# Kernel optimization log

Hardware: AMD Instinct MI355X
Metric: run time of the kernel (lower is better)

Reference implementation:

```python
import jax, jax.numpy as jnp
import numpy as np

N_ACTIVE = 32

def setup_inputs() -> dict:
    key = jax.random.key(0)
    ks = jax.random.split(key, 6)
    B, T, D, G, GD = 4, 2048, 2048, 4096, 256
    x = jax.random.normal(ks[0], (B, T, D), jnp.float32)
    Wc = jax.random.normal(ks[1], (G, D), jnp.float32) * (D ** -0.5)   # context_proj weight
    temperature = jnp.array(1.0, jnp.float32)
    genes = jax.random.normal(ks[2], (G, GD), jnp.float32) * 0.02      # dna_bank gene table
    Wd = jax.random.normal(ks[3], (D, GD), jnp.float32) * (GD ** -0.5) # gene_to_down weight
    Wu = jax.random.normal(ks[4], (D, GD), jnp.float32) * 0.02         # gene_to_up (zeros in init; random for testing)
    norm_w = jnp.ones((D,), jnp.float32)                               # RMSNorm weight
    scale = jnp.array(0.1, jnp.float32)
    return {"x": x, "Wc": Wc, "temperature": temperature, "genes": genes,
            "Wd": Wd, "Wu": Wu, "norm_w": norm_w, "scale": scale}

def reference(x, Wc, temperature, genes, Wd, Wu, norm_w, scale):
    # RMSNorm (torch default eps = finfo(dtype).eps, learnable elementwise weight)
    eps = jnp.finfo(x.dtype).eps
    xn = x * jax.lax.rsqrt(jnp.mean(x * x, axis=-1, keepdims=True) + eps) * norm_w
    # Expression: router logits over gene bank, temperature clamped at 0.1
    logits = jnp.einsum('btd,gd->btg', xn, Wc) / jnp.clip(temperature, 0.1)
    # top-k + scatter(-inf) + softmax == softmax over top-k values, zeros elsewhere
    top_vals, top_idx = jax.lax.top_k(logits, N_ACTIVE)        # (B,T,K)
    expr_w = jax.nn.softmax(top_vals, axis=-1)                 # (B,T,K)
    # dna_bank.express: weighted combination of genes. Only top-k entries are
    # nonzero, so gather + weighted sum is mathematically identical to the
    # dense (B,T,G)@(G,GD) combine the original materializes.
    expressed = jnp.einsum('btk,btkc->btc', expr_w, genes[top_idx])  # (B,T,GD)
    down = jnp.tanh(jnp.einsum('btc,dc->btd', expressed, Wd))
    up = jnp.einsum('btc,dc->btd', expressed, Wu)
    return down * xn * up * scale
```

## Files before the change

kernel.cpp:

```cpp
#include <hip/hip_runtime.h>
#include <math.h>

#define M_TOK 8192
#define D_DIM 2048
#define G_GENES 4096
#define GD_DIM 256
#define KSEL 32
#define NCAND 40
#define NSLICE 8

typedef float f32x4 __attribute__((ext_vector_type(4)));
typedef short bf16x8 __attribute__((ext_vector_type(8)));

__device__ __forceinline__ void async_copy16(const void* g, void* lds) {
  __builtin_amdgcn_global_load_lds((const __attribute__((address_space(1))) void*)g,
                                   (__attribute__((address_space(3))) void*)lds, 16, 0, 0);
}

__device__ __forceinline__ unsigned short f2bf(float f) {
  unsigned int u = __float_as_uint(f);
  unsigned int r = (u + 0x7fffu + ((u >> 16) & 1u)) >> 16;
  return (unsigned short)r;
}
__device__ __forceinline__ float bf2f(unsigned short h) {
  return __uint_as_float(((unsigned int)h) << 16);
}

__global__ __launch_bounds__(256) void k1_rmsnorm(const float* __restrict__ x,
                                                  const float* __restrict__ nw,
                                                  float* __restrict__ r_out,
                                                  unsigned short* __restrict__ xn_bf) {
  int t = blockIdx.x, tid = threadIdx.x;
  const float4* xr = (const float4*)(x + (size_t)t * D_DIM);
  float4 a = xr[tid], b = xr[tid + 256];
  double ss = (double)a.x*a.x + (double)a.y*a.y + (double)a.z*a.z + (double)a.w*a.w
            + (double)b.x*b.x + (double)b.y*b.y + (double)b.z*b.z + (double)b.w*b.w;
  for (int off = 32; off; off >>= 1) ss += __shfl_down(ss, off);
  __shared__ double sred[4];
  __shared__ float rshare;
  int lane = tid & 63, wv = tid >> 6;
  if (lane == 0) sred[wv] = ss;
  __syncthreads();
  if (tid == 0) {
    double tot = sred[0] + sred[1] + sred[2] + sred[3];
    float r = (float)(1.0 / sqrt(tot / (double)D_DIM + 1.1920928955078125e-7));
    rshare = r; r_out[t] = r;
  }
  __syncthreads();
  float r = rshare;
  const float4* nw4 = (const float4*)nw;
  float4 na = nw4[tid], nb = nw4[tid + 256];
  ushort4 oa, ob;
  oa.x = f2bf(a.x * r * na.x); oa.y = f2bf(a.y * r * na.y);
  oa.z = f2bf(a.z * r * na.z); oa.w = f2bf(a.w * r * na.w);
  ob.x = f2bf(b.x * r * nb.x); ob.y = f2bf(b.y * r * nb.y);
  ob.z = f2bf(b.z * r * nb.z); ob.w = f2bf(b.w * r * nb.w);
  ushort4* o4 = (ushort4*)(xn_bf + (size_t)t * D_DIM);
  o4[tid] = oa; o4[tid + 256] = ob;
}

__global__ __launch_bounds__(256) void k2_cvt(const float* __restrict__ w,
                                              unsigned short* __restrict__ wb) {
  size_t i = (size_t)blockIdx.x * 256 + threadIdx.x;
  const float4* w4 = (const float4*)w;
  float4 a = w4[2*i], b = w4[2*i+1];
  ushort4 oa, ob;
  oa.x = f2bf(a.x); oa.y = f2bf(a.y); oa.z = f2bf(a.z); oa.w = f2bf(a.w);
  ob.x = f2bf(b.x); ob.y = f2bf(b.y); ob.z = f2bf(b.z); ob.w = f2bf(b.w);
  ((ushort4*)wb)[2*i] = oa; ((ushort4*)wb)[2*i+1] = ob;
}

__global__ __launch_bounds__(256) void k2b_split(const float* __restrict__ wd,
                                                 const float* __restrict__ wu,
                                                 unsigned short* __restrict__ wdh,
                                                 unsigned short* __restrict__ wdl,
                                                 unsigned short* __restrict__ wuh,
                                                 unsigned short* __restrict__ wul) {
  const float* src = blockIdx.y ? wu : wd;
  unsigned short* dh = blockIdx.y ? wuh : wdh;
  unsigned short* dl = blockIdx.y ? wul : wdl;
  size_t i = (size_t)blockIdx.x * 256 + threadIdx.x;
  float4 v = ((const float4*)src)[i];
  ushort4 h, l;
  h.x = f2bf(v.x); l.x = f2bf(v.x - bf2f(h.x));
  h.y = f2bf(v.y); l.y = f2bf(v.y - bf2f(h.y));
  h.z = f2bf(v.z); l.z = f2bf(v.z - bf2f(h.z));
  h.w = f2bf(v.w); l.w = f2bf(v.w - bf2f(h.w));
  ((ushort4*)dh)[i] = h;
  ((ushort4*)dl)[i] = l;
}

__global__ __launch_bounds__(512, 1) void k3_gemm_logits(const unsigned short* __restrict__ A,
                                                         const unsigned short* __restrict__ B,
                                                         unsigned short* __restrict__ C) {
  __shared__ unsigned short As[4][256 * 32];
  __shared__ unsigned short Bs[4][256 * 32];
  const int tid = threadIdx.x;
  const int lane = tid & 63, wv = tid >> 6;
  const int wm = wv >> 2, wn = wv & 3;
  int lin = blockIdx.x;
  int swz = (lin & 7) * 64 + (lin >> 3);
  const int bm = swz & 31, bn = swz >> 5;

  const int grow = lane >> 2;
  const int gslot = (lane & 3) ^ ((lane >> 3) & 3);
  const unsigned short* agp = A + (size_t)(bm * 256 + wv * 32 + grow) * D_DIM + gslot * 8;
  const unsigned short* bgp = B + (size_t)(bn * 256 + wv * 32 + grow) * D_DIM + gslot * 8;
  const int fr = lane & 15;
  const int sw8 = (((lane >> 4) ^ ((lane >> 1) & 3))) * 8;

  f32x4 acc[8][4];
#pragma unroll
  for (int m = 0; m < 8; ++m)
#pragma unroll
    for (int n = 0; n < 4; ++n) acc[m][n] = (f32x4){0.f, 0.f, 0.f, 0.f};

#define STAGE_A3(t_) { const int b_ = (t_) & 3; const int kt_ = (t_) * 32;          \
    async_copy16(agp + kt_,              &As[b_][(wv * 32) * 32]);                   \
    async_copy16(agp + kt_ + 16 * D_DIM, &As[b_][(wv * 32 + 16) * 32]); }
#define STAGE_B3(t_) { const int b_ = (t_) & 3; const int kt_ = (t_) * 32;          \
    async_copy16(bgp + kt_,              &Bs[b_][(wv * 32) * 32]);                   \
    async_copy16(bgp + kt_ + 16 * D_DIM, &Bs[b_][(wv * 32 + 16) * 32]); }

#define READ_FRAGS(fa_, fb_, c_) {                                                   \
    const unsigned short* as_ = As[c_];                                              \
    const unsigned short* bs_ = Bs[c_];                                              \
    _Pragma("unroll") for (int n = 0; n < 4; ++n)                                    \
      fb_[n] = *(const bf16x8*)&bs_[(wn * 64 + n * 16 + fr) * 32 + sw8];             \
    _Pragma("unroll") for (int m = 0; m < 8; ++m)                                    \
      fa_[m] = *(const bf16x8*)&as_[(wm * 128 + m * 16 + fr) * 32 + sw8]; }

#define DO_MFMA(fa_, fb_) {                                                          \
    _Pragma("unroll") for (int m = 0; m < 4; ++m)                                    \
      _Pragma("unroll") for (int n = 0; n < 4; ++n)                                  \
        acc[m][n] = __builtin_amdgcn_mfma_f32_16x16x32_bf16(fa_[m], fb_[n], acc[m][n], 0, 0, 0); \
    _Pragma("unroll") for (int m = 0; m < 4; ++m)                                    \
      _Pragma("unroll") for (int n = 0; n < 4; ++n)                                  \
        acc[m + 4][n] = __builtin_amdgcn_mfma_f32_16x16x32_bf16(fa_[m + 4], fb_[n], acc[m + 4][n], 0, 0, 0); }

#define BODY(t_, CFA, CFB, NFA, NFB) {                                               \
    if ((t_) + 3 < 64) { STAGE_A3((t_) + 3); STAGE_B3((t_) + 3); }                   \
    READ_FRAGS(NFA, NFB, ((t_) + 1) & 3);                                            \
    asm volatile("s_waitcnt lgkmcnt(12)" ::: "memory");                              \
    __builtin_amdgcn_sched_barrier(0);                                               \
    __builtin_amdgcn_s_setprio(1);                                                   \
    DO_MFMA(CFA, CFB);                                                               \
    __builtin_amdgcn_s_setprio(0);                                                   \
    if ((t_) <= 60)      { asm volatile("s_waitcnt vmcnt(4)" ::: "memory"); }        \
    else if ((t_) == 61) { asm volatile("s_waitcnt vmcnt(0)" ::: "memory"); }        \
    __builtin_amdgcn_s_barrier(); }

  STAGE_A3(0); STAGE_B3(0);
  STAGE_A3(1); STAGE_B3(1);
  STAGE_A3(2); STAGE_B3(2);
  asm volatile("s_waitcnt vmcnt(4)" ::: "memory");
  __builtin_amdgcn_s_barrier();

  bf16x8 faA[8], fbA[4], faB[8], fbB[4];
  READ_FRAGS(faA, fbA, 0);

#pragma unroll 1
  for (int t = 0; t < 62; t += 2) {
    BODY(t,     faA, fbA, faB, fbB);
    BODY(t + 1, faB, fbB, faA, fbA);
  }
  BODY(62, faA, fbA, faB, fbB);
  asm volatile("s_waitcnt lgkmcnt(0)" ::: "memory");
  __builtin_amdgcn_sched_barrier(0);
  DO_MFMA(faB, fbB);

#undef BODY
#undef DO_MFMA
#undef READ_FRAGS
#undef STAGE_A3
#undef STAGE_B3

#pragma unroll
  for (int m = 0; m < 8; ++m)
#pragma unroll
    for (int n = 0; n < 4; ++n)
#pragma unroll
      for (int j = 0; j < 4; ++j) {
        int row = bm * 256 + wm * 128 + m * 16 + (lane >> 4) * 4 + j;
        int col = bn * 256 + wn * 64 + n * 16 + fr;
        C[(size_t)row * G_GENES + col] = f2bf(acc[m][n][j]);
      }
}

__global__ __launch_bounds__(256) void k4_topk(const unsigned short* __restrict__ L,
                                               int* __restrict__ cand) {
  int wv = threadIdx.x >> 6, lane = threadIdx.x & 63;
  int t = blockIdx.x * 4 + wv;
  const unsigned short* lp = L + (size_t)t * G_GENES;
  unsigned kp[32];
#pragma unroll
  for (int i = 0; i < 8; ++i) {
    uint4 raw = *(const uint4*)(lp + i * 512 + lane * 8);
    unsigned rr[4] = {raw.x, raw.y, raw.z, raw.w};
#pragma unroll
    for (int q = 0; q < 4; ++q) {
      unsigned r = rr[q];
      unsigned s = (r >> 15) & 0x00010001u;
      unsigned xm = 0x80008000u | (s * 0x7FFFu);
      kp[i * 4 + q] = r ^ xm;
    }
  }
  unsigned lo = 0, hi = 65536;
  while (hi - lo > 1u) {
    unsigned mid = (lo + hi) >> 1;
    int c = 0;
#pragma unroll
    for (int q = 0; q < 32; ++q) {
      c += __popcll(__ballot((kp[q] & 0xFFFFu) >= mid));
      c += __popcll(__ballot((kp[q] >> 16) >= mid));
    }
    if (c >= NCAND) lo = mid; else hi = mid;
  }
  const unsigned T = lo;
  unsigned long long below = (1ull << lane) - 1ull;
  int* outp = cand + (size_t)t * NCAND;
  int cnt = 0;
#pragma unroll
  for (int q = 0; q < 32; ++q) {
#pragma unroll
    for (int h = 0; h < 2; ++h) {
      unsigned key = h ? (kp[q] >> 16) : (kp[q] & 0xFFFFu);
      bool pred = key > T;
      unsigned long long m = __ballot(pred);
      if (pred) {
        int pos = cnt + (int)__popcll(m & below);
        outp[pos] = (q >> 2) * 512 + lane * 8 + (q & 3) * 2 + h;
      }
      cnt += (int)__popcll(m);
    }
  }
#pragma unroll 1
  for (int q = 0; q < 32 && cnt < NCAND; ++q) {
#pragma unroll
    for (int h = 0; h < 2; ++h) {
      unsigned key = h ? (kp[q] >> 16) : (kp[q] & 0xFFFFu);
      bool pred = key == T;
      unsigned long long m = __ballot(pred);
      if (pred) {
        int pos = cnt + (int)__popcll(m & below);
        if (pos < NCAND)
          outp[pos] = (q >> 2) * 512 + lane * 8 + (q & 3) * 2 + h;
      }
      cnt += (int)__popcll(m);
    }
  }
}

__global__ __launch_bounds__(256) void k5a_partial(const float* __restrict__ x,
                                                   const float* __restrict__ r,
                                                   const float* __restrict__ nw,
                                                   const float* __restrict__ Wc,
                                                   const int* __restrict__ cand,
                                                   double* __restrict__ part) {
  int bid = blockIdx.x;
  int slice = bid & 7;
  int group = bid >> 3;
  int wv = threadIdx.x >> 6, lane = threadIdx.x & 63;
  const int dbase = slice * 256;
  float4 nv = *(const float4*)(nw + dbase + lane * 4);
  bool b0 = (lane & 1) != 0, b1 = (lane & 2) != 0, b2 = (lane & 4) != 0;
#pragma unroll 1
  for (int tt = 0; tt < 2; ++tt) {
    int t = group * 8 + wv * 2 + tt;
    float rr = r[t];
    float4 xv = *(const float4*)(x + (size_t)t * D_DIM + dbase + lane * 4);
    float4 xl;
    xl.x = xv.x * rr * nv.x;
    xl.y = xv.y * rr * nv.y;
    xl.z = xv.z * rr * nv.z;
    xl.w = xv.w * rr * nv.w;
    int myg = cand[t * NCAND + (lane < NCAND ? lane : 0)];
    double* outp = part + ((size_t)t * NSLICE + slice) * NCAND;
#pragma unroll 1
    for (int j0 = 0; j0 < NCAND; j0 += 8) {
      float4 w[8];
#pragma unroll
      for (int c = 0; c < 8; ++c) {
        int g = __shfl(myg, j0 + c);
        w[c] = *(const float4*)(Wc + (size_t)g * D_DIM + dbase + lane * 4);
      }
      double s[8];
#pragma unroll
      for (int c = 0; c < 8; ++c)
        s[c] = ((double)xl.x * (double)w[c].x + (double)xl.y * (double)w[c].y)
             + ((double)xl.z * (double)w[c].z + (double)xl.w * (double)w[c].w);
      double u01 = b0 ? s[1] : s[0], t01 = b0 ? s[0] : s[1];
      double u23 = b0 ? s[3] : s[2], t23 = b0 ? s[2] : s[3];
      double u45 = b0 ? s[5] : s[4], t45 = b0 ? s[4] : s[5];
      double u67 = b0 ? s[7] : s[6], t67 = b0 ? s[6] : s[7];
      u01 += __shfl_xor(t01, 1);
      u23 += __shfl_xor(t23, 1);
      u45 += __shfl_xor(t45, 1);
      u67 += __shfl_xor(t67, 1);
      double v03 = b1 ? u23 : u01, t03 = b1 ? u01 : u23;
      double v47 = b1 ? u67 : u45, t47 = b1 ? u45 : u67;
      v03 += __shfl_xor(t03, 2);
      v47 += __shfl_xor(t47, 2);
      double wsum = b2 ? v47 : v03, t07 = b2 ? v03 : v47;
      wsum += __shfl_xor(t07, 4);
      wsum += __shfl_xor(wsum, 8);
      wsum += __shfl_xor(wsum, 16);
      wsum += __shfl_xor(wsum, 32);
      if (lane < 8) outp[j0 + lane] = wsum;
    }
  }
}

__global__ __launch_bounds__(256) void k6_express(const double* __restrict__ part,
                                                  const int* __restrict__ cand,
                                                  const float* __restrict__ genes,
                                                  const float* __restrict__ temp,
                                                  unsigned short* __restrict__ e_hi,
                                                  unsigned short* __restrict__ e_lo) {
  int t = blockIdx.x, tid = threadIdx.x;
  __shared__ double sval[NCAND];
  __shared__ int sidx[NCAND];
  __shared__ float sw[NCAND];
  float tclamp = fmaxf(temp[0], 0.1f);
  if (tid < NCAND) {
    const double* pp = part + (size_t)t * NSLICE * NCAND + tid;
    double v = 0.0;
#pragma unroll
    for (int s = 0; s < NSLICE; ++s) v += pp[s * NCAND];
    sval[tid] = v / (double)tclamp;
    sidx[tid] = cand[(size_t)t * NCAND + tid];
  }
  __syncthreads();
  if (tid < 64) {
    double v = (tid < NCAND) ? sval[tid] : -1.0e300;
    int gi = (tid < NCAND) ? sidx[tid] : 0x7fffffff;
    int rank = 0;
    for (int j = 0; j < NCAND; ++j) {
      double vj = sval[j]; int gj = sidx[j];
      if (vj > v || (vj == v && gj < gi)) rank++;
    }
    bool sel = (tid < NCAND) && (rank < KSEL);
    double vs = sel ? v : -1.0e300;
    double mx = vs;
    for (int off = 32; off; off >>= 1) { double o = __shfl_xor(mx, off); mx = fmax(mx, o); }
    double e = sel ? exp(v - mx) : 0.0;
    double ssum = e;
    for (int off = 32; off; off >>= 1) ssum += __shfl_xor(ssum, off);
    if (tid < NCAND) sw[tid] = (float)(e / ssum);
  }
  __syncthreads();
  float a0 = 0.f, a1 = 0.f, a2 = 0.f, a3 = 0.f;
#pragma unroll
  for (int k = 0; k < NCAND; k += 4) {
    a0 += sw[k]     * genes[(size_t)sidx[k]     * GD_DIM + tid];
    a1 += sw[k + 1] * genes[(size_t)sidx[k + 1] * GD_DIM + tid];
    a2 += sw[k + 2] * genes[(size_t)sidx[k + 2] * GD_DIM + tid];
    a3 += sw[k + 3] * genes[(size_t)sidx[k + 3] * GD_DIM + tid];
  }
  float acc = (a0 + a1) + (a2 + a3);
  unsigned short h = f2bf(acc);
  unsigned short l = f2bf(acc - bf2f(h));
  e_hi[(size_t)t * GD_DIM + tid] = h;
  e_lo[(size_t)t * GD_DIM + tid] = l;
}

__global__ __launch_bounds__(512, 1) void k7_mfma(const unsigned short* __restrict__ e_hi,
                                                  const unsigned short* __restrict__ e_lo,
                                                  const unsigned short* __restrict__ wdh,
                                                  const unsigned short* __restrict__ wdl,
                                                  const unsigned short* __restrict__ wuh,
                                                  const unsigned short* __restrict__ wul,
                                                  const float* __restrict__ x,
                                                  const float* __restrict__ r,
                                                  const float* __restrict__ nw,
                                                  const float* __restrict__ scale_p,
                                                  float* __restrict__ out) {
  __shared__ unsigned short L[3][6][128 * 32];
  const int tid = threadIdx.x;
  const int lane = tid & 63, wv = tid >> 6;
  const int wm = wv >> 2, wn = wv & 3;
  int lin = blockIdx.x;
  int swz = (lin & 7) * 128 + (lin >> 3);
  const int bm = swz & 63, bn = swz >> 6;

  const int grow = lane >> 2;
  const int gslot = (lane & 3) ^ ((lane >> 3) & 3);
  const int goff = gslot * 8;
  const unsigned short* ehp = e_hi + (size_t)(bm * 128 + wv * 16 + grow) * GD_DIM + goff;
  const unsigned short* elp = e_lo + (size_t)(bm * 128 + wv * 16 + grow) * GD_DIM + goff;
  const unsigned short* dhp = wdh + (size_t)(bn * 128 + wv * 16 + grow) * GD_DIM + goff;
  const unsigned short* dlp = wdl + (size_t)(bn * 128 + wv * 16 + grow) * GD_DIM + goff;
  const unsigned short* uhp = wuh + (size_t)(bn * 128 + wv * 16 + grow) * GD_DIM + goff;
  const unsigned short* ulp = wul + (size_t)(bn * 128 + wv * 16 + grow) * GD_DIM + goff;
  const int ldst = (wv * 16) * 32;

  const int fr = lane & 15;
  const int sw8 = ((lane >> 4) ^ ((lane >> 1) & 3)) * 8;

  f32x4 accD[4][2], accU[4][2];
#pragma unroll
  for (int m = 0; m < 4; ++m)
#pragma unroll
    for (int n = 0; n < 2; ++n) {
      accD[m][n] = (f32x4){0.f, 0.f, 0.f, 0.f};
      accU[m][n] = (f32x4){0.f, 0.f, 0.f, 0.f};
    }

#define STAGE7(t_) if ((t_) < 8) { const int b_ = (t_) % 3; const int kt_ = (t_) * 32; \
    async_copy16(ehp + kt_, &L[b_][0][ldst]); \
    async_copy16(elp + kt_, &L[b_][1][ldst]); \
    async_copy16(dhp + kt_, &L[b_][2][ldst]); \
    async_copy16(dlp + kt_, &L[b_][3][ldst]); \
    async_copy16(uhp + kt_, &L[b_][4][ldst]); \
    async_copy16(ulp + kt_, &L[b_][5][ldst]); }

  STAGE7(0); STAGE7(1);
  asm volatile("s_waitcnt vmcnt(6)" ::: "memory");
  __builtin_amdgcn_s_barrier();

#pragma unroll 1
  for (int t = 0; t < 8; ++t) {
    const int b = t % 3;
    bf16x8 fah[4], fal[4], fh[2], fl[2];
#pragma unroll
    for (int m = 0; m < 4; ++m) {
      int off = (wm * 64 + m * 16 + fr) * 32 + sw8;
      fah[m] = *(const bf16x8*)&L[b][0][off];
      fal[m] = *(const bf16x8*)&L[b][1][off];
    }
#pragma unroll
    for (int n = 0; n < 2; ++n) {
      int off = (wn * 32 + n * 16 + fr) * 32 + sw8;
      fh[n] = *(const bf16x8*)&L[b][2][off];
      fl[n] = *(const bf16x8*)&L[b][3][off];
    }
    STAGE7(t + 2);
    __builtin_amdgcn_s_barrier();
    asm volatile("s_waitcnt lgkmcnt(0)" ::: "memory");
    __builtin_amdgcn_sched_barrier(0);
    __builtin_amdgcn_s_setprio(1);
#pragma unroll
    for (int m = 0; m < 4; ++m)
#pragma unroll
      for (int n = 0; n < 2; ++n) {
        accD[m][n] = __builtin_amdgcn_mfma_f32_16x16x32_bf16(fah[m], fh[n], accD[m][n], 0, 0, 0);
        accD[m][n] = __builtin_amdgcn_mfma_f32_16x16x32_bf16(fah[m], fl[n], accD[m][n], 0, 0, 0);
        accD[m][n] = __builtin_amdgcn_mfma_f32_16x16x32_bf16(fal[m], fh[n], accD[m][n], 0, 0, 0);
      }
    __builtin_amdgcn_s_setprio(0);
    __builtin_amdgcn_s_barrier();
#pragma unroll
    for (int n = 0; n < 2; ++n) {
      int off = (wn * 32 + n * 16 + fr) * 32 + sw8;
      fh[n] = *(const bf16x8*)&L[b][4][off];
      fl[n] = *(const bf16x8*)&L[b][5][off];
    }
    __builtin_amdgcn_s_barrier();
    asm volatile("s_waitcnt lgkmcnt(0)" ::: "memory");
    __builtin_amdgcn_sched_barrier(0);
    __builtin_amdgcn_s_setprio(1);
#pragma unroll
    for (int m = 0; m < 4; ++m)
#pragma unroll
      for (int n = 0; n < 2; ++n) {
        accU[m][n] = __builtin_amdgcn_mfma_f32_16x16x32_bf16(fah[m], fh[n], accU[m][n], 0, 0, 0);
        accU[m][n] = __builtin_amdgcn_mfma_f32_16x16x32_bf16(fah[m], fl[n], accU[m][n], 0, 0, 0);
        accU[m][n] = __builtin_amdgcn_mfma_f32_16x16x32_bf16(fal[m], fh[n], accU[m][n], 0, 0, 0);
      }
    __builtin_amdgcn_s_setprio(0);
    if (t <= 5)      { asm volatile("s_waitcnt vmcnt(6)" ::: "memory"); }
    else if (t == 6) { asm volatile("s_waitcnt vmcnt(0)" ::: "memory"); }
    __builtin_amdgcn_s_barrier();
  }
#undef STAGE7

  float sc = scale_p[0];
#pragma unroll
  for (int m = 0; m < 4; ++m)
#pragma unroll
    for (int j = 0; j < 4; ++j) {
      int token = bm * 128 + wm * 64 + m * 16 + (lane >> 4) * 4 + j;
      float rr = r[token];
#pragma unroll
      for (int n = 0; n < 2; ++n) {
        int d = bn * 128 + wn * 32 + n * 16 + fr;
        float xn = x[(size_t)token * D_DIM + d] * rr * nw[d];
        out[(size_t)token * D_DIM + d] = tanhf(accD[m][n][j]) * xn * accU[m][n][j] * sc;
      }
    }
}

extern "C" void kernel_launch(void* const* d_in, const int* in_sizes, int n_in,
                              void* d_out, int out_size, void* d_ws, size_t ws_size,
                              hipStream_t stream) {
  const float* x       = (const float*)d_in[0];
  const float* Wc      = (const float*)d_in[1];
  const float* temp    = (const float*)d_in[2];
  const float* genes   = (const float*)d_in[3];
  const float* Wd      = (const float*)d_in[4];
  const float* Wu      = (const float*)d_in[5];
  const float* nw      = (const float*)d_in[6];
  const float* scale_p = (const float*)d_in[7];

  char* ws = (char*)d_ws;
  float* r_buf          = (float*)ws;
  unsigned short* xn_bf = (unsigned short*)(ws + 65536);
  unsigned short* wc_bf = (unsigned short*)(ws + 65536 + (size_t)M_TOK * D_DIM * 2);
  char* p = ws + 65536 + (size_t)M_TOK * D_DIM * 2 + (size_t)G_GENES * D_DIM * 2;
  int* cand    = (int*)p;                       p += (size_t)M_TOK * NCAND * 4;
  p += (size_t)M_TOK * NCAND * 8;
  unsigned short* e_hi = (unsigned short*)p;    p += (size_t)M_TOK * GD_DIM * 2;
  unsigned short* e_lo = (unsigned short*)p;

  unsigned short* wdh = (unsigned short*)(ws + 65536);
  unsigned short* wdl = wdh + (size_t)D_DIM * GD_DIM;
  unsigned short* wuh = wdl + (size_t)D_DIM * GD_DIM;
  unsigned short* wul = wuh + (size_t)D_DIM * GD_DIM;
  double* part = (double*)(ws + 65536 + 4ull * D_DIM * GD_DIM * 2);

  unsigned short* logits_bf = (unsigned short*)d_out;

  k1_rmsnorm<<<dim3(M_TOK), dim3(256), 0, stream>>>(x, nw, r_buf, xn_bf);
  k2_cvt<<<dim3((G_GENES * D_DIM) / (256 * 8)), dim3(256), 0, stream>>>(Wc, wc_bf);
  k3_gemm_logits<<<dim3((M_TOK / 256) * (G_GENES / 256)), dim3(512), 0, stream>>>(xn_bf, wc_bf, logits_bf);
  k4_topk<<<dim3(M_TOK / 4), dim3(256), 0, stream>>>(logits_bf, cand);
  k2b_split<<<dim3((D_DIM * GD_DIM) / (256 * 4), 2), dim3(256), 0, stream>>>(Wd, Wu, wdh, wdl, wuh, wul);
  k5a_partial<<<dim3(M_TOK), dim3(256), 0, stream>>>(x, r_buf, nw, Wc, cand, part);
  k6_express<<<dim3(M_TOK), dim3(256), 0, stream>>>(part, cand, genes, temp, e_hi, e_lo);
  k7_mfma<<<dim3((M_TOK / 128) * (D_DIM / 128)), dim3(512), 0, stream>>>(e_hi, e_lo, wdh, wdl, wuh, wul,
                                                                         x, r_buf, nw, scale_p, (float*)d_out);
}
```

Before: 490.0 us.

## Switch logits GEMM to double-buffered LDS and request higher occupancy

Reduces the logits GEMM shared-memory pipeline from four stages with register-level fragment prefetch to a simple two-stage double buffer, and raises the launch bound's minimum blocks per CU from 1 to 4. The intent is to rely on more resident blocks to hide memory latency instead of deep software pipelining. The higher occupancy request constrains registers per thread well below what the 128-float accumulator tile needs, risking spills, and the shallower pipeline waits on each global load every iteration.

```diff
diff --git a/kernel.cpp b/kernel.cpp
--- a/kernel.cpp
+++ b/kernel.cpp
@@ -90,11 +90,11 @@
   ((ushort4*)dl)[i] = l;
 }
 
-__global__ __launch_bounds__(512, 1) void k3_gemm_logits(const unsigned short* __restrict__ A,
+__global__ __launch_bounds__(512, 4) void k3_gemm_logits(const unsigned short* __restrict__ A,
                                                          const unsigned short* __restrict__ B,
                                                          unsigned short* __restrict__ C) {
-  __shared__ unsigned short As[4][256 * 32];
-  __shared__ unsigned short Bs[4][256 * 32];
+  __shared__ unsigned short As[2][256 * 32];
+  __shared__ unsigned short Bs[2][256 * 32];
   const int tid = threadIdx.x;
   const int lane = tid & 63, wv = tid >> 6;
   const int wm = wv >> 2, wn = wv & 3;
@@ -115,65 +115,46 @@
 #pragma unroll
     for (int n = 0; n < 4; ++n) acc[m][n] = (f32x4){0.f, 0.f, 0.f, 0.f};
 
-#define STAGE_A3(t_) { const int b_ = (t_) & 3; const int kt_ = (t_) * 32;          \
+#define STAGE_AB(t_, b_) { const int kt_ = (t_) * 32;                                \
     async_copy16(agp + kt_,              &As[b_][(wv * 32) * 32]);                   \
-    async_copy16(agp + kt_ + 16 * D_DIM, &As[b_][(wv * 32 + 16) * 32]); }
-#define STAGE_B3(t_) { const int b_ = (t_) & 3; const int kt_ = (t_) * 32;          \
+    async_copy16(agp + kt_ + 16 * D_DIM, &As[b_][(wv * 32 + 16) * 32]);              \
     async_copy16(bgp + kt_,              &Bs[b_][(wv * 32) * 32]);                   \
     async_copy16(bgp + kt_ + 16 * D_DIM, &Bs[b_][(wv * 32 + 16) * 32]); }
 
-#define READ_FRAGS(fa_, fb_, c_) {                                                   \
-    const unsigned short* as_ = As[c_];                                              \
-    const unsigned short* bs_ = Bs[c_];                                              \
+#define BODY(t_) {                                                                   \
+    const int cb_ = (t_) & 1;                                                        \
+    if ((t_) + 1 < 64) STAGE_AB((t_) + 1, cb_ ^ 1);                                  \
+    const unsigned short* as_ = As[cb_];                                             \
+    const unsigned short* bs_ = Bs[cb_];                                             \
+    bf16x8 fa_[8], fb_[4];                                                           \
     _Pragma("unroll") for (int n = 0; n < 4; ++n)                                    \
       fb_[n] = *(const bf16x8*)&bs_[(wn * 64 + n * 16 + fr) * 32 + sw8];             \
     _Pragma("unroll") for (int m = 0; m < 8; ++m)                                    \
-      fa_[m] = *(const bf16x8*)&as_[(wm * 128 + m * 16 + fr) * 32 + sw8]; }
-
-#define DO_MFMA(fa_, fb_) {                                                          \
+      fa_[m] = *(const bf16x8*)&as_[(wm * 128 + m * 16 + fr) * 32 + sw8];            \
+    asm volatile("s_waitcnt lgkmcnt(0)" ::: "memory");                               \
+    __builtin_amdgcn_sched_barrier(0);                                               \
+    __builtin_amdgcn_s_setprio(1);                                                   \
     _Pragma("unroll") for (int m = 0; m < 4; ++m)                                    \
       _Pragma("unroll") for (int n = 0; n < 4; ++n)                                  \
         acc[m][n] = __builtin_amdgcn_mfma_f32_16x16x32_bf16(fa_[m], fb_[n], acc[m][n], 0, 0, 0); \
     _Pragma("unroll") for (int m = 0; m < 4; ++m)                                    \
       _Pragma("unroll") for (int n = 0; n < 4; ++n)                                  \
-        acc[m + 4][n] = __builtin_amdgcn_mfma_f32_16x16x32_bf16(fa_[m + 4], fb_[n], acc[m + 4][n], 0, 0, 0); }
-
-#define BODY(t_, CFA, CFB, NFA, NFB) {                                               \
-    if ((t_) + 3 < 64) { STAGE_A3((t_) + 3); STAGE_B3((t_) + 3); }                   \
-    READ_FRAGS(NFA, NFB, ((t_) + 1) & 3);                                            \
-    asm volatile("s_waitcnt lgkmcnt(12)" ::: "memory");                              \
-    __builtin_amdgcn_sched_barrier(0);                                               \
-    __builtin_amdgcn_s_setprio(1);                                                   \
-    DO_MFMA(CFA, CFB);                                                               \
+        acc[m + 4][n] = __builtin_amdgcn_mfma_f32_16x16x32_bf16(fa_[m + 4], fb_[n], acc[m + 4][n], 0, 0, 0); \
     __builtin_amdgcn_s_setprio(0);                                                   \
-    if ((t_) <= 60)      { asm volatile("s_waitcnt vmcnt(4)" ::: "memory"); }        \
-    else if ((t_) == 61) { asm volatile("s_waitcnt vmcnt(0)" ::: "memory"); }        \
+    asm volatile("s_waitcnt vmcnt(0)" ::: "memory");                                 \
     __builtin_amdgcn_s_barrier(); }
 
-  STAGE_A3(0); STAGE_B3(0);
-  STAGE_A3(1); STAGE_B3(1);
-  STAGE_A3(2); STAGE_B3(2);
-  asm volatile("s_waitcnt vmcnt(4)" ::: "memory");
+  STAGE_AB(0, 0);
+  asm volatile("s_waitcnt vmcnt(0)" ::: "memory");
   __builtin_amdgcn_s_barrier();
 
-  bf16x8 faA[8], fbA[4], faB[8], fbB[4];
-  READ_FRAGS(faA, fbA, 0);
-
 #pragma unroll 1
-  for (int t = 0; t < 62; t += 2) {
-    BODY(t,     faA, fbA, faB, fbB);
-    BODY(t + 1, faB, fbB, faA, fbA);
-  }
-  BODY(62, faA, fbA, faB, fbB);
-  asm volatile("s_waitcnt lgkmcnt(0)" ::: "memory");
-  __builtin_amdgcn_sched_barrier(0);
-  DO_MFMA(faB, fbB);
-
+  for (int t = 0; t < 64; t += 2) {
+    BODY(t);
+    BODY(t + 1);
+  }
 #undef BODY
-#undef DO_MFMA
-#undef READ_FRAGS
-#undef STAGE_A3
-#undef STAGE_B3
+#undef STAGE_AB
 
 #pragma unroll
   for (int m = 0; m < 8; ++m)
```

Result: slower. 1.787 ms (+264.8%).
